# Kernel optimization log

Hardware: AMD Instinct MI355X
Metric: run time of the kernel (lower is better)

Reference implementation:

```python
import jax, jax.numpy as jnp
import numpy as np

N_FP, N_WORD, DIM, LAYERS = 100000, 10000, 32, 3
N_ATOMS, N_WORDS_SEQ = 8192, 4096


def setup_inputs() -> dict:
    key = jax.random.key(0)
    ks = jax.random.split(key, 7)
    return {
        "fingerprints": jax.random.randint(ks[0], (N_ATOMS,), 0, N_FP),
        "adjacency": jax.random.uniform(ks[1], (N_ATOMS, N_ATOMS), dtype=jnp.float32),
        "words": jax.random.randint(ks[2], (N_WORDS_SEQ,), 0, N_WORD),
        "emb_fp": jax.random.normal(ks[3], (N_FP, DIM), dtype=jnp.float32) * 0.02,
        "emb_word": jax.random.normal(ks[4], (N_WORD, DIM), dtype=jnp.float32) * 0.02,
        "Wg": jax.random.normal(ks[5], (LAYERS, DIM, DIM), dtype=jnp.float32) / np.sqrt(DIM),
        "bg": jax.random.normal(ks[6], (LAYERS, DIM), dtype=jnp.float32) * 0.01,
    }


def reference(fingerprints, adjacency, words, emb_fp, emb_word, Wg, bg):
    # Compound vector with GNN: xs <- xs + A @ relu(xs @ W_i + b_i), per layer.
    xs = emb_fp[fingerprints]  # [N, dim]

    def layer(x, wb):
        W, b = wb
        hs = jax.nn.relu(x @ W + b)          # [N, dim]
        return x + adjacency @ hs, None      # dense adjacency matmul + residual

    xs, _ = jax.lax.scan(layer, xs, (Wg, bg))
    compound_vector = xs[None]               # [1, N, dim] (torch.unsqueeze(xs, 0))

    # Protein word embedding lookup (encoder/decoder are external modules).
    word_vectors = emb_word[words]           # [S, dim]
    return compound_vector, word_vectors
```

## Files before the change

kernel.cpp:

```cpp
#include <hip/hip_runtime.h>
#include <hip/hip_bf16.h>
#include <cstdint>
#include <cstddef>

#define NATOMS 8192
#define DIM 32
#define NSEQ 4096
#define KSPLIT 16
#define BM 256
#define BK 32
#define KPB (NATOMS / KSPLIT)
#define NT (KPB / BK)

typedef __attribute__((address_space(1))) const void GV;
typedef __attribute__((address_space(3))) void LV;
using bf16x8 = __attribute__((ext_vector_type(8))) short;
using f32x4  = __attribute__((ext_vector_type(4))) float;

__device__ __forceinline__ void async16(void* lds, const void* g) {
  __builtin_amdgcn_global_load_lds((GV*)g, (LV*)lds, 16, 0, 0);
}
__device__ __forceinline__ void async16nt(void* lds, const void* g) {
  __builtin_amdgcn_global_load_lds((GV*)g, (LV*)lds, 16, 0, 2);
}
__device__ __forceinline__ uint32_t pkbf(float lo, float hi) {
  union { __hip_bfloat16 b[2]; uint32_t u; } v;
  v.b[0] = __float2bfloat16(lo);
  v.b[1] = __float2bfloat16(hi);
  return v.u;
}
__device__ __forceinline__ float ubf(ushort u) {
  union { ushort u; __hip_bfloat16 b; } v;
  v.u = u;
  return __bfloat162float(v.b);
}
union U8 { uint32_t u[4]; bf16x8 v; };

__device__ __forceinline__ int aslot(int r, int g) { return g ^ ((r >> 1) & 3); }
__device__ __forceinline__ int hslot(int n, int g) { return g ^ ((n >> 1) & 3); }

__global__ __launch_bounds__(256, 2)
void cpi_gemm1(const float* __restrict__ A, const ushort* __restrict__ hT,
               float* __restrict__ P, ushort* __restrict__ Abf) {
  __shared__ float  Ab[2][BM * BK];
  __shared__ ushort Hb[2][DIM * BK];

  const int tid  = threadIdx.x;
  const int wave = tid >> 6;
  const int lane = tid & 63;
  const int l15  = lane & 15;
  const int l4   = lane >> 4;
  const int rb   = blockIdx.x & 31;
  const int ks   = blockIdx.x >> 5;
  const int row0 = rb * BM;
  const int k0   = ks * KPB;

  f32x4 acc[4][2];
#pragma unroll
  for (int rt = 0; rt < 4; ++rt)
#pragma unroll
    for (int ct = 0; ct < 2; ++ct) acc[rt][ct] = {0.f, 0.f, 0.f, 0.f};

  auto stage = [&](int buf, int t) {
    const int kb = k0 + t * BK;
#pragma unroll
    for (int i = 0; i < 8; ++i) {
      const int D = (wave * 8 + i) * 64 + lane;
      const int r = D >> 3;
      const int c = D & 7;
      const float* src =
          A + (size_t)(row0 + r) * NATOMS + kb + ((c ^ (r & 7)) << 2);
      async16nt(&Ab[buf][(wave * 8 + i) * 256], src);
    }
    if (wave < 2) {
      const int E = wave * 64 + lane;
      const int n = E >> 2;
      const int s = E & 3;
      const ushort* src = hT + (size_t)n * NATOMS + kb + (hslot(n, s) << 3);
      async16(&Hb[buf][wave * 512], src);
    }
  };

  stage(0, 0);
  asm volatile("s_waitcnt vmcnt(0)" ::: "memory");
  __syncthreads();

  int cur = 0;
#pragma unroll 1
  for (int t = 0; t < NT; ++t) {
    if (t + 1 < NT) stage(cur ^ 1, t + 1);

    const float*  Ac = &Ab[cur][0];
    const ushort* Hc = &Hb[cur][0];

    bf16x8 av[4];
#pragma unroll
    for (int rt = 0; rt < 4; ++rt) {
      const int r = wave * 64 + rt * 16 + l15;
      const float4 f0 =
          *(const float4*)(Ac + r * 32 + (((2 * l4) ^ (r & 7)) << 2));
      const float4 f1 =
          *(const float4*)(Ac + r * 32 + (((2 * l4 + 1) ^ (r & 7)) << 2));
      U8 u;
      u.u[0] = pkbf(f0.x, f0.y);
      u.u[1] = pkbf(f0.z, f0.w);
      u.u[2] = pkbf(f1.x, f1.y);
      u.u[3] = pkbf(f1.z, f1.w);
      av[rt] = u.v;
    }
    bf16x8 bv[2];
#pragma unroll
    for (int ct = 0; ct < 2; ++ct) {
      const int n = ct * 16 + l15;
      bv[ct] = *(const bf16x8*)(Hc + n * 32 + (hslot(n, l4) << 3));
    }

    ushort* Tb = Abf + (((size_t)ks * 32 + rb) * 16 + t) * (BM * BK);
#pragma unroll
    for (int rt = 0; rt < 4; ++rt) {
      const int r = wave * 64 + rt * 16 + l15;
      *(bf16x8*)(Tb + r * 32 + (aslot(r, l4) << 3)) = av[rt];
    }

#pragma unroll
    for (int rt = 0; rt < 4; ++rt)
#pragma unroll
      for (int ct = 0; ct < 2; ++ct)
        acc[rt][ct] = __builtin_amdgcn_mfma_f32_16x16x32_bf16(
            av[rt], bv[ct], acc[rt][ct], 0, 0, 0);

    asm volatile("s_waitcnt vmcnt(4)" ::: "memory");
    __syncthreads();
    cur ^= 1;
  }

  float* Pp = P + ((((size_t)ks * 32 + rb) * 4 + wave) * 8) * 256;
#pragma unroll
  for (int rt = 0; rt < 4; ++rt)
#pragma unroll
    for (int ct = 0; ct < 2; ++ct)
      *(f32x4*)(Pp + (rt * 2 + ct) * 256 + lane * 4) = acc[rt][ct];
}

__global__ __launch_bounds__(256, 2)
void cpi_gemm2(const ushort* __restrict__ Abf, const ushort* __restrict__ hT,
               ushort* __restrict__ Pb, const int ntA) {
  __shared__ ushort Ab[3][BM * BK];
  __shared__ ushort Hb[3][DIM * BK];

  const int tid  = threadIdx.x;
  const int wave = tid >> 6;
  const int lane = tid & 63;
  const int l15  = lane & 15;
  const int l4   = lane >> 4;
  const int rb   = blockIdx.x & 31;
  const int ks   = blockIdx.x >> 5;
  const int k0   = ks * KPB;

  f32x4 acc[4][2];
#pragma unroll
  for (int rt = 0; rt < 4; ++rt)
#pragma unroll
    for (int ct = 0; ct < 2; ++ct) acc[rt][ct] = {0.f, 0.f, 0.f, 0.f};

  auto stage = [&](int buf, int t) {
    const ushort* Tb = Abf + (((size_t)ks * 32 + rb) * 16 + t) * (BM * BK);
#pragma unroll
    for (int i = 0; i < 4; ++i) {
      const ushort* src = Tb + ((wave * 4 + i) * 64 + lane) * 8;
      void* dst = &Ab[buf][(wave * 4 + i) * 512];
      if (ntA)
        async16nt(dst, src);
      else
        async16(dst, src);
    }
    if (wave < 2) {
      const int kb = k0 + t * BK;
      const int E = wave * 64 + lane;
      const int n = E >> 2;
      const int s = E & 3;
      const ushort* src = hT + (size_t)n * NATOMS + kb + (hslot(n, s) << 3);
      async16(&Hb[buf][wave * 512], src);
    }
  };

  stage(0, 0);
  stage(1, 1);

#pragma unroll 1
  for (int t = 0; t < NT; ++t) {
    if (t + 1 < NT) {
      if (wave < 2)
        asm volatile("s_waitcnt vmcnt(5)" ::: "memory");
      else
        asm volatile("s_waitcnt vmcnt(4)" ::: "memory");
    } else {
      asm volatile("s_waitcnt vmcnt(0)" ::: "memory");
    }
    __syncthreads();
    if (t + 2 < NT) stage((t + 2) % 3, t + 2);

    const ushort* Ac = &Ab[t % 3][0];
    const ushort* Hc = &Hb[t % 3][0];

    bf16x8 av[4], bv[2];
#pragma unroll
    for (int rt = 0; rt < 4; ++rt) {
      const int r = wave * 64 + rt * 16 + l15;
      av[rt] = *(const bf16x8*)(Ac + r * 32 + (aslot(r, l4) << 3));
    }
#pragma unroll
    for (int ct = 0; ct < 2; ++ct) {
      const int n = ct * 16 + l15;
      bv[ct] = *(const bf16x8*)(Hc + n * 32 + (hslot(n, l4) << 3));
    }

#pragma unroll
    for (int rt = 0; rt < 4; ++rt)
#pragma unroll
      for (int ct = 0; ct < 2; ++ct)
        acc[rt][ct] = __builtin_amdgcn_mfma_f32_16x16x32_bf16(
            av[rt], bv[ct], acc[rt][ct], 0, 0, 0);
  }

  ushort* Pp = Pb + ((((size_t)ks * 32 + rb) * 4 + wave) * 8) * 256;
#pragma unroll
  for (int rt = 0; rt < 4; ++rt)
#pragma unroll
    for (int ct = 0; ct < 2; ++ct) {
      uint2 u;
      u.x = pkbf(acc[rt][ct].x, acc[rt][ct].y);
      u.y = pkbf(acc[rt][ct].z, acc[rt][ct].w);
      *(uint2*)(Pp + (rt * 2 + ct) * 256 + lane * 4) = u;
    }
}

__global__ __launch_bounds__(256)
void cpi_front(const int* __restrict__ fp, const float* __restrict__ embfp,
               const float* __restrict__ W, const float* __restrict__ b,
               float* __restrict__ xs, ushort* __restrict__ hT,
               const int* __restrict__ words, const float* __restrict__ embw,
               float* __restrict__ wout) {
  if (blockIdx.x >= NATOMS / 8) {
    const int i = (blockIdx.x - NATOMS / 8) * 256 + threadIdx.x;
    wout[i] = embw[(size_t)words[i >> 5] * DIM + (i & 31)];
    return;
  }
  __shared__ float xsl[8][DIM];
  __shared__ float Wl[DIM][DIM];
  const int tid = threadIdx.x;
  const int col = tid & 31;
  const int r8  = tid >> 5;
  const int row = blockIdx.x * 8 + r8;
  const int f   = fp[row];
  const float v = embfp[(size_t)f * DIM + col];
  xs[(size_t)row * DIM + col] = v;
  xsl[r8][col] = v;
#pragma unroll
  for (int i = 0; i < 4; ++i) {
    const int idx = tid + i * 256;
    ((float*)Wl)[idx] = W[idx];
  }
  __syncthreads();
  float a = b[col];
#pragma unroll
  for (int d = 0; d < DIM; ++d) a += xsl[r8][d] * Wl[d][col];
  union { __hip_bfloat16 bb; ushort u; } cv;
  cv.bb = __float2bfloat16(fmaxf(a, 0.f));
  hT[(size_t)col * NATOMS + row] = cv.u;
}

__global__ __launch_bounds__(256)
void cpi_reduce_h(const float* __restrict__ P, const ushort* __restrict__ Pb,
                  const int p_is_bf16, const float* __restrict__ W,
                  const float* __restrict__ b, float* __restrict__ xs,
                  ushort* __restrict__ hT, const int compute_h) {
  __shared__ float xsl[8][DIM];
  __shared__ float Wl[DIM][DIM];
  const int tid = threadIdx.x;
  const int col = tid & 31;
  const int r8  = tid >> 5;
  const int row = blockIdx.x * 8 + r8;
  const size_t off = (size_t)row * DIM + col;
  float s = xs[off];
  {
    const int rbv = row >> 8, rr = row & 255;
    const int w = rr >> 6, rr6 = rr & 63;
    const int rt = rr6 >> 4, q4 = (rr6 >> 2) & 3, i = rr6 & 3;
    const int ct = col >> 4, lane = q4 * 16 + (col & 15);
    const int base = ((rbv * 4 + w) * 8 + rt * 2 + ct) * 256 + lane * 4 + i;
    if (p_is_bf16) {
#pragma unroll
      for (int k = 0; k < KSPLIT; ++k)
        s += ubf(Pb[(size_t)k * (NATOMS * DIM) + base]);
    } else {
#pragma unroll
      for (int k = 0; k < KSPLIT; ++k)
        s += __builtin_nontemporal_load(&P[(size_t)k * (NATOMS * DIM) + base]);
    }
  }
  xs[off] = s;
  if (compute_h) {
    xsl[r8][col] = s;
#pragma unroll
    for (int i = 0; i < 4; ++i) {
      const int idx = tid + i * 256;
      ((float*)Wl)[idx] = W[idx];
    }
    __syncthreads();
    float a = b[col];
#pragma unroll
    for (int d = 0; d < DIM; ++d) a += xsl[r8][d] * Wl[d][col];
    union { __hip_bfloat16 bb; ushort u; } cv;
    cv.bb = __float2bfloat16(fmaxf(a, 0.f));
    hT[(size_t)col * NATOMS + row] = cv.u;
  }
}

extern "C" void kernel_launch(void* const* d_in, const int* in_sizes, int n_in,
                              void* d_out, int out_size, void* d_ws, size_t ws_size,
                              hipStream_t stream) {
  const int*   fp    = (const int*)d_in[0];
  const float* adj   = (const float*)d_in[1];
  const int*   words = (const int*)d_in[2];
  const float* embfp = (const float*)d_in[3];
  const float* embw  = (const float*)d_in[4];
  const float* Wg    = (const float*)d_in[5];
  const float* bg    = (const float*)d_in[6];

  float* out = (float*)d_out;
  float* xs  = out;
  float* wv  = out + NATOMS * DIM;

  float*  P   = (float*)d_ws;
  ushort* Pb  = (ushort*)P;
  ushort* Abf = (ushort*)(P + (size_t)KSPLIT * NATOMS * DIM);
  ushort* hT  = Abf + (size_t)NATOMS * NATOMS;

  cpi_front<<<dim3(NATOMS / 8 + NSEQ * DIM / 256), dim3(256), 0, stream>>>(
      fp, embfp, Wg, bg, xs, hT, words, embw, wv);

  cpi_gemm1<<<dim3(512), dim3(256), 0, stream>>>(adj, hT, P, Abf);
  cpi_reduce_h<<<dim3(NATOMS / 8), dim3(256), 0, stream>>>(
      P, Pb, 0, Wg + DIM * DIM, bg + DIM, xs, hT, 1);

  cpi_gemm2<<<dim3(512), dim3(256), 0, stream>>>(Abf, hT, Pb, 0);
  cpi_reduce_h<<<dim3(NATOMS / 8), dim3(256), 0, stream>>>(
      P, Pb, 1, Wg + 2 * DIM * DIM, bg + 2 * DIM, xs, hT, 1);

  cpi_gemm2<<<dim3(512), dim3(256), 0, stream>>>(Abf, hT, Pb, 1);
  cpi_reduce_h<<<dim3(NATOMS / 8), dim3(256), 0, stream>>>(
      P, Pb, 1, Wg, bg, xs, hT, 0);
}
```

Measured before the change: 141.4 us.

## Fuse split-K reduction and next-layer h compute into GEMM via last-block atomics

Removes the three separate reduce_h launches. Each GEMM block now bumps a per-row-block atomic counter, and the last of the KSPLIT blocks for that row block sums the partials, updates xs, and computes the next layer's relu(xW+b) into a ping-pong hT buffer. This saves launch overhead and the extra pass over the partials, but leaves the reduction tail to only 32 blocks, which serialises that work. Counters are zeroed by an extra block in the front kernel.

```diff
diff --git a/kernel.cpp b/kernel.cpp
--- a/kernel.cpp
+++ b/kernel.cpp
@@ -11,11 +11,13 @@
 #define BK 32
 #define KPB (NATOMS / KSPLIT)
 #define NT (KPB / BK)
+#define FRONT_NB (NATOMS / 8 + NSEQ * DIM / 256)
 
 typedef __attribute__((address_space(1))) const void GV;
 typedef __attribute__((address_space(3))) void LV;
 using bf16x8 = __attribute__((ext_vector_type(8))) short;
 using f32x4  = __attribute__((ext_vector_type(4))) float;
+using u32x2  = __attribute__((ext_vector_type(2))) unsigned int;
 
 __device__ __forceinline__ void async16(void* lds, const void* g) {
   __builtin_amdgcn_global_load_lds((GV*)g, (LV*)lds, 16, 0, 0);
@@ -34,16 +36,48 @@
   v.u = u;
   return __bfloat162float(v.b);
 }
+__device__ __forceinline__ ushort bfr(float a) {
+  union { __hip_bfloat16 b; ushort u; } v;
+  v.b = __float2bfloat16(a);
+  return v.u;
+}
 union U8 { uint32_t u[4]; bf16x8 v; };
 
 __device__ __forceinline__ int aslot(int r, int g) { return g ^ ((r >> 1) & 3); }
 __device__ __forceinline__ int hslot(int n, int g) { return g ^ ((n >> 1) & 3); }
 
+__device__ __forceinline__ void h_tail(const float* xsl, const float* Wl,
+                                       const float* bn, ushort* hTout,
+                                       int row0, int tid) {
+  float wcol[DIM];
+  const int c = tid & 31;
+#pragma unroll
+  for (int d = 0; d < DIM; ++d) wcol[d] = Wl[d * DIM + c];
+  const float bb = bn[c];
+#pragma unroll 1
+  for (int it = 0; it < 32; ++it) {
+    const int r = it * 8 + (tid >> 5);
+    float a = bb;
+    const f32x4* xr = (const f32x4*)(xsl + r * DIM);
+#pragma unroll
+    for (int q = 0; q < 8; ++q) {
+      f32x4 x4 = xr[q];
+      a += x4.x * wcol[q * 4] + x4.y * wcol[q * 4 + 1] +
+           x4.z * wcol[q * 4 + 2] + x4.w * wcol[q * 4 + 3];
+    }
+    hTout[(size_t)c * NATOMS + row0 + r] = bfr(fmaxf(a, 0.f));
+  }
+}
+
 __global__ __launch_bounds__(256, 2)
-void cpi_gemm1(const float* __restrict__ A, const ushort* __restrict__ hT,
-               float* __restrict__ P, ushort* __restrict__ Abf) {
+void cpi_gemm1(const float* __restrict__ A, const ushort* __restrict__ hTin,
+               float* __restrict__ P, ushort* __restrict__ Abf,
+               int* __restrict__ cnt, const float* __restrict__ Wn,
+               const float* __restrict__ bn, float* __restrict__ xs,
+               ushort* __restrict__ hTout) {
   __shared__ float  Ab[2][BM * BK];
   __shared__ ushort Hb[2][DIM * BK];
+  __shared__ int lastFlag;
 
   const int tid  = threadIdx.x;
   const int wave = tid >> 6;
@@ -76,7 +110,7 @@
       const int E = wave * 64 + lane;
       const int n = E >> 2;
       const int s = E & 3;
-      const ushort* src = hT + (size_t)n * NATOMS + kb + (hslot(n, s) << 3);
+      const ushort* src = hTin + (size_t)n * NATOMS + kb + (hslot(n, s) << 3);
       async16(&Hb[buf][wave * 512], src);
     }
   };
@@ -140,13 +174,59 @@
 #pragma unroll
     for (int ct = 0; ct < 2; ++ct)
       *(f32x4*)(Pp + (rt * 2 + ct) * 256 + lane * 4) = acc[rt][ct];
+
+  asm volatile("s_waitcnt vmcnt(0)" ::: "memory");
+  __syncthreads();
+  if (tid == 0) {
+    int c = __hip_atomic_fetch_add(&cnt[rb], 1, __ATOMIC_ACQ_REL,
+                                   __HIP_MEMORY_SCOPE_AGENT);
+    lastFlag = (c == KSPLIT - 1);
+  }
+  __syncthreads();
+  if (!lastFlag) return;
+
+  float* xsl = (float*)&Ab[0][0];
+  float* Wl  = xsl + 256 * DIM;
+  for (int i = tid; i < DIM * DIM; i += 256) Wl[i] = Wn[i];
+
+  const int colq = lane & 15, rq = lane >> 4;
+#pragma unroll
+  for (int f = 0; f < 8; ++f) {
+    const size_t base = ((size_t)(rb * 4 + wave) * 8 + f) * 256 + lane * 4;
+    const int rt = f >> 1, ct = f & 1;
+    f32x4 a4;
+#pragma unroll
+    for (int i = 0; i < 4; ++i) {
+      const int row = wave * 64 + rt * 16 + rq * 4 + i;
+      a4[i] = xs[(size_t)(row0 + row) * DIM + ct * 16 + colq];
+    }
+#pragma unroll
+    for (int k = 0; k < KSPLIT; ++k) {
+      f32x4 v = __builtin_nontemporal_load(
+          (const f32x4*)(P + (size_t)k * (NATOMS * DIM) + base));
+      a4.x += v.x; a4.y += v.y; a4.z += v.z; a4.w += v.w;
+    }
+#pragma unroll
+    for (int i = 0; i < 4; ++i) {
+      const int row = wave * 64 + rt * 16 + rq * 4 + i;
+      const int col = ct * 16 + colq;
+      xs[(size_t)(row0 + row) * DIM + col] = a4[i];
+      xsl[row * DIM + col] = a4[i];
+    }
+  }
+  __syncthreads();
+  h_tail(xsl, Wl, bn, hTout, row0, tid);
 }
 
 __global__ __launch_bounds__(256, 2)
-void cpi_gemm2(const ushort* __restrict__ Abf, const ushort* __restrict__ hT,
-               ushort* __restrict__ Pb, const int ntA) {
+void cpi_gemm2(const ushort* __restrict__ Abf, const ushort* __restrict__ hTin,
+               ushort* __restrict__ Pb, const int ntA, int* __restrict__ cnt,
+               const float* __restrict__ Wn, const float* __restrict__ bn,
+               float* __restrict__ xs, ushort* __restrict__ hTout,
+               const int doH) {
   __shared__ ushort Ab[3][BM * BK];
   __shared__ ushort Hb[3][DIM * BK];
+  __shared__ int lastFlag;
 
   const int tid  = threadIdx.x;
   const int wave = tid >> 6;
@@ -155,6 +235,7 @@
   const int l4   = lane >> 4;
   const int rb   = blockIdx.x & 31;
   const int ks   = blockIdx.x >> 5;
+  const int row0 = rb * BM;
   const int k0   = ks * KPB;
 
   f32x4 acc[4][2];
@@ -179,7 +260,7 @@
       const int E = wave * 64 + lane;
       const int n = E >> 2;
       const int s = E & 3;
-      const ushort* src = hT + (size_t)n * NATOMS + kb + (hslot(n, s) << 3);
+      const ushort* src = hTin + (size_t)n * NATOMS + kb + (hslot(n, s) << 3);
       async16(&Hb[buf][wave * 512], src);
     }
   };
@@ -228,11 +309,59 @@
   for (int rt = 0; rt < 4; ++rt)
 #pragma unroll
     for (int ct = 0; ct < 2; ++ct) {
-      uint2 u;
+      u32x2 u;
       u.x = pkbf(acc[rt][ct].x, acc[rt][ct].y);
       u.y = pkbf(acc[rt][ct].z, acc[rt][ct].w);
-      *(uint2*)(Pp + (rt * 2 + ct) * 256 + lane * 4) = u;
-    }
+      *(u32x2*)(Pp + (rt * 2 + ct) * 256 + lane * 4) = u;
+    }
+
+  asm volatile("s_waitcnt vmcnt(0)" ::: "memory");
+  __syncthreads();
+  if (tid == 0) {
+    int c = __hip_atomic_fetch_add(&cnt[rb], 1, __ATOMIC_ACQ_REL,
+                                   __HIP_MEMORY_SCOPE_AGENT);
+    lastFlag = (c == KSPLIT - 1);
+  }
+  __syncthreads();
+  if (!lastFlag) return;
+
+  float* xsl = (float*)&Ab[0][0];
+  float* Wl  = xsl + 256 * DIM;
+  if (doH)
+    for (int i = tid; i < DIM * DIM; i += 256) Wl[i] = Wn[i];
+
+  const int colq = lane & 15, rq = lane >> 4;
+#pragma unroll
+  for (int f = 0; f < 8; ++f) {
+    const size_t base = ((size_t)(rb * 4 + wave) * 8 + f) * 256 + lane * 4;
+    const int rt = f >> 1, ct = f & 1;
+    f32x4 a4;
+#pragma unroll
+    for (int i = 0; i < 4; ++i) {
+      const int row = wave * 64 + rt * 16 + rq * 4 + i;
+      a4[i] = xs[(size_t)(row0 + row) * DIM + ct * 16 + colq];
+    }
+#pragma unroll
+    for (int k = 0; k < KSPLIT; ++k) {
+      u32x2 v = __builtin_nontemporal_load(
+          (const u32x2*)(Pb + (size_t)k * (NATOMS * DIM) + base));
+      a4.x += ubf((ushort)(v.x & 0xffff));
+      a4.y += ubf((ushort)(v.x >> 16));
+      a4.z += ubf((ushort)(v.y & 0xffff));
+      a4.w += ubf((ushort)(v.y >> 16));
+    }
+#pragma unroll
+    for (int i = 0; i < 4; ++i) {
+      const int row = wave * 64 + rt * 16 + rq * 4 + i;
+      const int col = ct * 16 + colq;
+      xs[(size_t)(row0 + row) * DIM + col] = a4[i];
+      if (doH) xsl[row * DIM + col] = a4[i];
+    }
+  }
+  if (doH) {
+    __syncthreads();
+    h_tail(xsl, Wl, bn, hTout, row0, tid);
+  }
 }
 
 __global__ __launch_bounds__(256)
@@ -240,7 +369,11 @@
                const float* __restrict__ W, const float* __restrict__ b,
                float* __restrict__ xs, ushort* __restrict__ hT,
                const int* __restrict__ words, const float* __restrict__ embw,
-               float* __restrict__ wout) {
+               float* __restrict__ wout, int* __restrict__ cnt) {
+  if (blockIdx.x == FRONT_NB) {
+    if (threadIdx.x < 96) cnt[threadIdx.x] = 0;
+    return;
+  }
   if (blockIdx.x >= NATOMS / 8) {
     const int i = (blockIdx.x - NATOMS / 8) * 256 + threadIdx.x;
     wout[i] = embw[(size_t)words[i >> 5] * DIM + (i & 31)];
@@ -265,56 +398,7 @@
   float a = b[col];
 #pragma unroll
   for (int d = 0; d < DIM; ++d) a += xsl[r8][d] * Wl[d][col];
-  union { __hip_bfloat16 bb; ushort u; } cv;
-  cv.bb = __float2bfloat16(fmaxf(a, 0.f));
-  hT[(size_t)col * NATOMS + row] = cv.u;
-}
-
-__global__ __launch_bounds__(256)
-void cpi_reduce_h(const float* __restrict__ P, const ushort* __restrict__ Pb,
-                  const int p_is_bf16, const float* __restrict__ W,
-                  const float* __restrict__ b, float* __restrict__ xs,
-                  ushort* __restrict__ hT, const int compute_h) {
-  __shared__ float xsl[8][DIM];
-  __shared__ float Wl[DIM][DIM];
-  const int tid = threadIdx.x;
-  const int col = tid & 31;
-  const int r8  = tid >> 5;
-  const int row = blockIdx.x * 8 + r8;
-  const size_t off = (size_t)row * DIM + col;
-  float s = xs[off];
-  {
-    const int rbv = row >> 8, rr = row & 255;
-    const int w = rr >> 6, rr6 = rr & 63;
-    const int rt = rr6 >> 4, q4 = (rr6 >> 2) & 3, i = rr6 & 3;
-    const int ct = col >> 4, lane = q4 * 16 + (col & 15);
-    const int base = ((rbv * 4 + w) * 8 + rt * 2 + ct) * 256 + lane * 4 + i;
-    if (p_is_bf16) {
-#pragma unroll
-      for (int k = 0; k < KSPLIT; ++k)
-        s += ubf(Pb[(size_t)k * (NATOMS * DIM) + base]);
-    } else {
-#pragma unroll
-      for (int k = 0; k < KSPLIT; ++k)
-        s += __builtin_nontemporal_load(&P[(size_t)k * (NATOMS * DIM) + base]);
-    }
-  }
-  xs[off] = s;
-  if (compute_h) {
-    xsl[r8][col] = s;
-#pragma unroll
-    for (int i = 0; i < 4; ++i) {
-      const int idx = tid + i * 256;
-      ((float*)Wl)[idx] = W[idx];
-    }
-    __syncthreads();
-    float a = b[col];
-#pragma unroll
-    for (int d = 0; d < DIM; ++d) a += xsl[r8][d] * Wl[d][col];
-    union { __hip_bfloat16 bb; ushort u; } cv;
-    cv.bb = __float2bfloat16(fmaxf(a, 0.f));
-    hT[(size_t)col * NATOMS + row] = cv.u;
-  }
+  hT[(size_t)col * NATOMS + row] = bfr(fmaxf(a, 0.f));
 }
 
 extern "C" void kernel_launch(void* const* d_in, const int* in_sizes, int n_in,
@@ -335,20 +419,19 @@
   float*  P   = (float*)d_ws;
   ushort* Pb  = (ushort*)P;
   ushort* Abf = (ushort*)(P + (size_t)KSPLIT * NATOMS * DIM);
-  ushort* hT  = Abf + (size_t)NATOMS * NATOMS;
-
-  cpi_front<<<dim3(NATOMS / 8 + NSEQ * DIM / 256), dim3(256), 0, stream>>>(
-      fp, embfp, Wg, bg, xs, hT, words, embw, wv);
-
-  cpi_gemm1<<<dim3(512), dim3(256), 0, stream>>>(adj, hT, P, Abf);
-  cpi_reduce_h<<<dim3(NATOMS / 8), dim3(256), 0, stream>>>(
-      P, Pb, 0, Wg + DIM * DIM, bg + DIM, xs, hT, 1);
-
-  cpi_gemm2<<<dim3(512), dim3(256), 0, stream>>>(Abf, hT, Pb, 0);
-  cpi_reduce_h<<<dim3(NATOMS / 8), dim3(256), 0, stream>>>(
-      P, Pb, 1, Wg + 2 * DIM * DIM, bg + 2 * DIM, xs, hT, 1);
-
-  cpi_gemm2<<<dim3(512), dim3(256), 0, stream>>>(Abf, hT, Pb, 1);
-  cpi_reduce_h<<<dim3(NATOMS / 8), dim3(256), 0, stream>>>(
-      P, Pb, 1, Wg, bg, xs, hT, 0);
-}
+  ushort* hTa = Abf + (size_t)NATOMS * NATOMS;
+  ushort* hTb = hTa + (size_t)DIM * NATOMS;
+  int*    cnt = (int*)(hTb + (size_t)DIM * NATOMS);
+
+  cpi_front<<<dim3(FRONT_NB + 1), dim3(256), 0, stream>>>(
+      fp, embfp, Wg, bg, xs, hTa, words, embw, wv, cnt);
+
+  cpi_gemm1<<<dim3(512), dim3(256), 0, stream>>>(
+      adj, hTa, P, Abf, cnt, Wg + DIM * DIM, bg + DIM, xs, hTb);
+
+  cpi_gemm2<<<dim3(512), dim3(256), 0, stream>>>(
+      Abf, hTb, Pb, 0, cnt + 32, Wg + 2 * DIM * DIM, bg + 2 * DIM, xs, hTa, 1);
+
+  cpi_gemm2<<<dim3(512), dim3(256), 0, stream>>>(
+      Abf, hTa, Pb, 1, cnt + 64, Wg, bg, xs, hTb, 0);
+}
```

New measurement: 201.1 us. 1.42x slower.

## Fuse all GNN layers into one persistent kernel with grid barriers

Applied to the files above, without the earlier changes.

Replaces the seven kernel launches (front, gemm1, gemm2 and the reduce kernels) with one persistent 512-block kernel. Software grid barriers built on atomics separate the phases. Each block keeps its own xs rows in registers across the reduce phases, and hT is double-buffered so a phase never overwrites the hT it is reading. This is meant to remove launch gaps and the xs round trips through global memory. The risks are that all 512 blocks must be co-resident (two per CU) or the barrier deadlocks, each barrier adds spin and atomic cost, and the large shared buffer may limit occupancy.

```diff
diff --git a/kernel.cpp b/kernel.cpp
--- a/kernel.cpp
+++ b/kernel.cpp
@@ -11,11 +11,13 @@
 #define BK 32
 #define KPB (NATOMS / KSPLIT)
 #define NT (KPB / BK)
+#define NBLK 512
 
 typedef __attribute__((address_space(1))) const void GV;
 typedef __attribute__((address_space(3))) void LV;
 using bf16x8 = __attribute__((ext_vector_type(8))) short;
 using f32x4  = __attribute__((ext_vector_type(4))) float;
+using u32x2  = __attribute__((ext_vector_type(2))) unsigned int;
 
 __device__ __forceinline__ void async16(void* lds, const void* g) {
   __builtin_amdgcn_global_load_lds((GV*)g, (LV*)lds, 16, 0, 0);
@@ -34,129 +36,38 @@
   v.u = u;
   return __bfloat162float(v.b);
 }
+__device__ __forceinline__ ushort bfr(float a) {
+  union { __hip_bfloat16 b; ushort u; } v;
+  v.b = __float2bfloat16(a);
+  return v.u;
+}
 union U8 { uint32_t u[4]; bf16x8 v; };
 
 __device__ __forceinline__ int aslot(int r, int g) { return g ^ ((r >> 1) & 3); }
 __device__ __forceinline__ int hslot(int n, int g) { return g ^ ((n >> 1) & 3); }
 
-__global__ __launch_bounds__(256, 2)
-void cpi_gemm1(const float* __restrict__ A, const ushort* __restrict__ hT,
-               float* __restrict__ P, ushort* __restrict__ Abf) {
-  __shared__ float  Ab[2][BM * BK];
-  __shared__ ushort Hb[2][DIM * BK];
-
-  const int tid  = threadIdx.x;
-  const int wave = tid >> 6;
-  const int lane = tid & 63;
-  const int l15  = lane & 15;
-  const int l4   = lane >> 4;
-  const int rb   = blockIdx.x & 31;
-  const int ks   = blockIdx.x >> 5;
-  const int row0 = rb * BM;
-  const int k0   = ks * KPB;
-
-  f32x4 acc[4][2];
-#pragma unroll
-  for (int rt = 0; rt < 4; ++rt)
-#pragma unroll
-    for (int ct = 0; ct < 2; ++ct) acc[rt][ct] = {0.f, 0.f, 0.f, 0.f};
-
-  auto stage = [&](int buf, int t) {
-    const int kb = k0 + t * BK;
-#pragma unroll
-    for (int i = 0; i < 8; ++i) {
-      const int D = (wave * 8 + i) * 64 + lane;
-      const int r = D >> 3;
-      const int c = D & 7;
-      const float* src =
-          A + (size_t)(row0 + r) * NATOMS + kb + ((c ^ (r & 7)) << 2);
-      async16nt(&Ab[buf][(wave * 8 + i) * 256], src);
-    }
-    if (wave < 2) {
-      const int E = wave * 64 + lane;
-      const int n = E >> 2;
-      const int s = E & 3;
-      const ushort* src = hT + (size_t)n * NATOMS + kb + (hslot(n, s) << 3);
-      async16(&Hb[buf][wave * 512], src);
-    }
-  };
-
-  stage(0, 0);
-  asm volatile("s_waitcnt vmcnt(0)" ::: "memory");
+__device__ __forceinline__ void gridbar(int* cnt, int* gen, int tid) {
   __syncthreads();
-
-  int cur = 0;
-#pragma unroll 1
-  for (int t = 0; t < NT; ++t) {
-    if (t + 1 < NT) stage(cur ^ 1, t + 1);
-
-    const float*  Ac = &Ab[cur][0];
-    const ushort* Hc = &Hb[cur][0];
-
-    bf16x8 av[4];
-#pragma unroll
-    for (int rt = 0; rt < 4; ++rt) {
-      const int r = wave * 64 + rt * 16 + l15;
-      const float4 f0 =
-          *(const float4*)(Ac + r * 32 + (((2 * l4) ^ (r & 7)) << 2));
-      const float4 f1 =
-          *(const float4*)(Ac + r * 32 + (((2 * l4 + 1) ^ (r & 7)) << 2));
-      U8 u;
-      u.u[0] = pkbf(f0.x, f0.y);
-      u.u[1] = pkbf(f0.z, f0.w);
-      u.u[2] = pkbf(f1.x, f1.y);
-      u.u[3] = pkbf(f1.z, f1.w);
-      av[rt] = u.v;
-    }
-    bf16x8 bv[2];
-#pragma unroll
-    for (int ct = 0; ct < 2; ++ct) {
-      const int n = ct * 16 + l15;
-      bv[ct] = *(const bf16x8*)(Hc + n * 32 + (hslot(n, l4) << 3));
-    }
-
-    ushort* Tb = Abf + (((size_t)ks * 32 + rb) * 16 + t) * (BM * BK);
-#pragma unroll
-    for (int rt = 0; rt < 4; ++rt) {
-      const int r = wave * 64 + rt * 16 + l15;
-      *(bf16x8*)(Tb + r * 32 + (aslot(r, l4) << 3)) = av[rt];
-    }
-
-#pragma unroll
-    for (int rt = 0; rt < 4; ++rt)
-#pragma unroll
-      for (int ct = 0; ct < 2; ++ct)
-        acc[rt][ct] = __builtin_amdgcn_mfma_f32_16x16x32_bf16(
-            av[rt], bv[ct], acc[rt][ct], 0, 0, 0);
-
-    asm volatile("s_waitcnt vmcnt(4)" ::: "memory");
-    __syncthreads();
-    cur ^= 1;
-  }
-
-  float* Pp = P + ((((size_t)ks * 32 + rb) * 4 + wave) * 8) * 256;
-#pragma unroll
-  for (int rt = 0; rt < 4; ++rt)
-#pragma unroll
-    for (int ct = 0; ct < 2; ++ct)
-      *(f32x4*)(Pp + (rt * 2 + ct) * 256 + lane * 4) = acc[rt][ct];
-}
-
-__global__ __launch_bounds__(256, 2)
-void cpi_gemm2(const ushort* __restrict__ Abf, const ushort* __restrict__ hT,
-               ushort* __restrict__ Pb, const int ntA) {
-  __shared__ ushort Ab[3][BM * BK];
-  __shared__ ushort Hb[3][DIM * BK];
-
-  const int tid  = threadIdx.x;
-  const int wave = tid >> 6;
-  const int lane = tid & 63;
-  const int l15  = lane & 15;
-  const int l4   = lane >> 4;
-  const int rb   = blockIdx.x & 31;
-  const int ks   = blockIdx.x >> 5;
-  const int k0   = ks * KPB;
-
+  if (tid == 0) {
+    int g = __hip_atomic_load(gen, __ATOMIC_RELAXED, __HIP_MEMORY_SCOPE_AGENT);
+    if (__hip_atomic_fetch_add(cnt, 1, __ATOMIC_ACQ_REL,
+                               __HIP_MEMORY_SCOPE_AGENT) == NBLK - 1) {
+      __hip_atomic_store(cnt, 0, __ATOMIC_RELAXED, __HIP_MEMORY_SCOPE_AGENT);
+      __hip_atomic_store(gen, g ^ 1, __ATOMIC_RELEASE,
+                         __HIP_MEMORY_SCOPE_AGENT);
+    } else {
+      while (__hip_atomic_load(gen, __ATOMIC_ACQUIRE,
+                               __HIP_MEMORY_SCOPE_AGENT) == g)
+        __builtin_amdgcn_s_sleep(8);
+    }
+  }
+  __syncthreads();
+}
+
+__device__ __forceinline__ void gemm2_body(
+    const ushort* __restrict__ Abf, const ushort* __restrict__ hTin,
+    ushort* __restrict__ Pb, int ntA, ushort* AbB, ushort* HbU, int tid,
+    int wave, int lane, int l15, int l4, int rb, int ks, int k0) {
   f32x4 acc[4][2];
 #pragma unroll
   for (int rt = 0; rt < 4; ++rt)
@@ -168,7 +79,7 @@
 #pragma unroll
     for (int i = 0; i < 4; ++i) {
       const ushort* src = Tb + ((wave * 4 + i) * 64 + lane) * 8;
-      void* dst = &Ab[buf][(wave * 4 + i) * 512];
+      void* dst = AbB + buf * 8192 + (wave * 4 + i) * 512;
       if (ntA)
         async16nt(dst, src);
       else
@@ -179,8 +90,8 @@
       const int E = wave * 64 + lane;
       const int n = E >> 2;
       const int s = E & 3;
-      const ushort* src = hT + (size_t)n * NATOMS + kb + (hslot(n, s) << 3);
-      async16(&Hb[buf][wave * 512], src);
+      const ushort* src = hTin + (size_t)n * NATOMS + kb + (hslot(n, s) << 3);
+      async16(HbU + buf * 1024 + wave * 512, src);
     }
   };
 
@@ -200,8 +111,8 @@
     __syncthreads();
     if (t + 2 < NT) stage((t + 2) % 3, t + 2);
 
-    const ushort* Ac = &Ab[t % 3][0];
-    const ushort* Hc = &Hb[t % 3][0];
+    const ushort* Ac = AbB + (t % 3) * 8192;
+    const ushort* Hc = HbU + (t % 3) * 1024;
 
     bf16x8 av[4], bv[2];
 #pragma unroll
@@ -228,68 +139,32 @@
   for (int rt = 0; rt < 4; ++rt)
 #pragma unroll
     for (int ct = 0; ct < 2; ++ct) {
-      uint2 u;
+      u32x2 u;
       u.x = pkbf(acc[rt][ct].x, acc[rt][ct].y);
       u.y = pkbf(acc[rt][ct].z, acc[rt][ct].w);
-      *(uint2*)(Pp + (rt * 2 + ct) * 256 + lane * 4) = u;
-    }
-}
-
-__global__ __launch_bounds__(256)
-void cpi_front(const int* __restrict__ fp, const float* __restrict__ embfp,
-               const float* __restrict__ W, const float* __restrict__ b,
-               float* __restrict__ xs, ushort* __restrict__ hT,
-               const int* __restrict__ words, const float* __restrict__ embw,
-               float* __restrict__ wout) {
-  if (blockIdx.x >= NATOMS / 8) {
-    const int i = (blockIdx.x - NATOMS / 8) * 256 + threadIdx.x;
-    wout[i] = embw[(size_t)words[i >> 5] * DIM + (i & 31)];
-    return;
-  }
-  __shared__ float xsl[8][DIM];
-  __shared__ float Wl[DIM][DIM];
-  const int tid = threadIdx.x;
+      *(u32x2*)(Pp + (rt * 2 + ct) * 256 + lane * 4) = u;
+    }
+}
+
+__device__ __forceinline__ void reduce_body(
+    const float* __restrict__ P, const ushort* __restrict__ Pb, int isbf,
+    const float* __restrict__ Wn, const float* __restrict__ bn,
+    ushort* __restrict__ hTout, int doH, float* xsr, float* xsl, float* Wl,
+    int row0r, int tid) {
   const int col = tid & 31;
-  const int r8  = tid >> 5;
-  const int row = blockIdx.x * 8 + r8;
-  const int f   = fp[row];
-  const float v = embfp[(size_t)f * DIM + col];
-  xs[(size_t)row * DIM + col] = v;
-  xsl[r8][col] = v;
-#pragma unroll
-  for (int i = 0; i < 4; ++i) {
-    const int idx = tid + i * 256;
-    ((float*)Wl)[idx] = W[idx];
-  }
-  __syncthreads();
-  float a = b[col];
-#pragma unroll
-  for (int d = 0; d < DIM; ++d) a += xsl[r8][d] * Wl[d][col];
-  union { __hip_bfloat16 bb; ushort u; } cv;
-  cv.bb = __float2bfloat16(fmaxf(a, 0.f));
-  hT[(size_t)col * NATOMS + row] = cv.u;
-}
-
-__global__ __launch_bounds__(256)
-void cpi_reduce_h(const float* __restrict__ P, const ushort* __restrict__ Pb,
-                  const int p_is_bf16, const float* __restrict__ W,
-                  const float* __restrict__ b, float* __restrict__ xs,
-                  ushort* __restrict__ hT, const int compute_h) {
-  __shared__ float xsl[8][DIM];
-  __shared__ float Wl[DIM][DIM];
-  const int tid = threadIdx.x;
-  const int col = tid & 31;
-  const int r8  = tid >> 5;
-  const int row = blockIdx.x * 8 + r8;
-  const size_t off = (size_t)row * DIM + col;
-  float s = xs[off];
-  {
-    const int rbv = row >> 8, rr = row & 255;
-    const int w = rr >> 6, rr6 = rr & 63;
+  if (doH)
+    for (int i = tid; i < DIM * DIM; i += 256) Wl[i] = Wn[i];
+#pragma unroll
+  for (int rr = 0; rr < 2; ++rr) {
+    const int lr = (tid >> 5) + rr * 8;
+    const int row = row0r + lr;
+    const int rbv = row >> 8, r255 = row & 255;
+    const int w = r255 >> 6, rr6 = r255 & 63;
     const int rt = rr6 >> 4, q4 = (rr6 >> 2) & 3, i = rr6 & 3;
     const int ct = col >> 4, lane = q4 * 16 + (col & 15);
     const int base = ((rbv * 4 + w) * 8 + rt * 2 + ct) * 256 + lane * 4 + i;
-    if (p_is_bf16) {
+    float s = xsr[rr];
+    if (isbf) {
 #pragma unroll
       for (int k = 0; k < KSPLIT; ++k)
         s += ubf(Pb[(size_t)k * (NATOMS * DIM) + base]);
@@ -298,22 +173,192 @@
       for (int k = 0; k < KSPLIT; ++k)
         s += __builtin_nontemporal_load(&P[(size_t)k * (NATOMS * DIM) + base]);
     }
-  }
-  xs[off] = s;
-  if (compute_h) {
-    xsl[r8][col] = s;
-#pragma unroll
-    for (int i = 0; i < 4; ++i) {
-      const int idx = tid + i * 256;
-      ((float*)Wl)[idx] = W[idx];
-    }
+    xsr[rr] = s;
+    if (doH) xsl[lr * DIM + col] = s;
+  }
+  if (doH) {
     __syncthreads();
-    float a = b[col];
-#pragma unroll
-    for (int d = 0; d < DIM; ++d) a += xsl[r8][d] * Wl[d][col];
-    union { __hip_bfloat16 bb; ushort u; } cv;
-    cv.bb = __float2bfloat16(fmaxf(a, 0.f));
-    hT[(size_t)col * NATOMS + row] = cv.u;
+    float wc[DIM];
+#pragma unroll
+    for (int d = 0; d < DIM; ++d) wc[d] = Wl[d * DIM + col];
+    const float bb = bn[col];
+#pragma unroll
+    for (int rr = 0; rr < 2; ++rr) {
+      const int lr = (tid >> 5) + rr * 8;
+      float a = bb;
+#pragma unroll
+      for (int d = 0; d < DIM; ++d) a += xsl[lr * DIM + d] * wc[d];
+      hTout[(size_t)col * NATOMS + row0r + lr] = bfr(fmaxf(a, 0.f));
+    }
+  }
+}
+
+__global__ __launch_bounds__(256, 2)
+void cpi_mega(const int* __restrict__ fp, const float* __restrict__ adj,
+              const int* __restrict__ words, const float* __restrict__ embfp,
+              const float* __restrict__ embw, const float* __restrict__ Wg,
+              const float* __restrict__ bg, float* __restrict__ out,
+              float* __restrict__ P, ushort* __restrict__ Pb,
+              ushort* __restrict__ Abf, ushort* __restrict__ hTa,
+              ushort* __restrict__ hTb, int* __restrict__ bar) {
+  __shared__ __align__(16) char smem[71680];
+  float*  AbF = (float*)smem;
+  ushort* AbB = (ushort*)smem;
+  ushort* HbU = (ushort*)(smem + 65536);
+  float*  xsl = (float*)smem;
+  float*  Wl  = (float*)(smem + 4096);
+
+  const int tid   = threadIdx.x;
+  const int bid   = blockIdx.x;
+  const int wave  = tid >> 6;
+  const int lane  = tid & 63;
+  const int l15   = lane & 15;
+  const int l4    = lane >> 4;
+  const int rb    = bid & 31;
+  const int ks    = bid >> 5;
+  const int row0g = rb * BM;
+  const int k0    = ks * KPB;
+  const int row0r = bid * 16;
+  const int col   = tid & 31;
+
+  float xsr[2];
+
+  {
+    const int wi = bid * 256 + tid;
+    out[NATOMS * DIM + wi] = embw[(size_t)words[wi >> 5] * DIM + (wi & 31)];
+    for (int i = tid; i < DIM * DIM; i += 256) Wl[i] = Wg[i];
+#pragma unroll
+    for (int rr = 0; rr < 2; ++rr) {
+      const int lr = (tid >> 5) + rr * 8;
+      const float v = embfp[(size_t)fp[row0r + lr] * DIM + col];
+      xsr[rr] = v;
+      xsl[lr * DIM + col] = v;
+    }
+    __syncthreads();
+    float wc[DIM];
+#pragma unroll
+    for (int d = 0; d < DIM; ++d) wc[d] = Wl[d * DIM + col];
+    const float bb = bg[col];
+#pragma unroll
+    for (int rr = 0; rr < 2; ++rr) {
+      const int lr = (tid >> 5) + rr * 8;
+      float a = bb;
+#pragma unroll
+      for (int d = 0; d < DIM; ++d) a += xsl[lr * DIM + d] * wc[d];
+      hTa[(size_t)col * NATOMS + row0r + lr] = bfr(fmaxf(a, 0.f));
+    }
+  }
+  gridbar(bar, bar + 1, tid);
+
+  {
+    f32x4 acc[4][2];
+#pragma unroll
+    for (int rt = 0; rt < 4; ++rt)
+#pragma unroll
+      for (int ct = 0; ct < 2; ++ct) acc[rt][ct] = {0.f, 0.f, 0.f, 0.f};
+
+    auto stage = [&](int buf, int t) {
+      const int kb = k0 + t * BK;
+#pragma unroll
+      for (int i = 0; i < 8; ++i) {
+        const int D = (wave * 8 + i) * 64 + lane;
+        const int r = D >> 3;
+        const int c = D & 7;
+        const float* src =
+            adj + (size_t)(row0g + r) * NATOMS + kb + ((c ^ (r & 7)) << 2);
+        async16nt(AbF + buf * 8192 + (wave * 8 + i) * 256, src);
+      }
+      if (wave < 2) {
+        const int E = wave * 64 + lane;
+        const int n = E >> 2;
+        const int s = E & 3;
+        const ushort* src =
+            hTa + (size_t)n * NATOMS + kb + (hslot(n, s) << 3);
+        async16(HbU + buf * 1024 + wave * 512, src);
+      }
+    };
+
+    stage(0, 0);
+    asm volatile("s_waitcnt vmcnt(0)" ::: "memory");
+    __syncthreads();
+
+    int cur = 0;
+#pragma unroll 1
+    for (int t = 0; t < NT; ++t) {
+      if (t + 1 < NT) stage(cur ^ 1, t + 1);
+
+      const float*  Ac = AbF + cur * 8192;
+      const ushort* Hc = HbU + cur * 1024;
+
+      bf16x8 av[4];
+#pragma unroll
+      for (int rt = 0; rt < 4; ++rt) {
+        const int r = wave * 64 + rt * 16 + l15;
+        const float4 f0 =
+            *(const float4*)(Ac + r * 32 + (((2 * l4) ^ (r & 7)) << 2));
+        const float4 f1 =
+            *(const float4*)(Ac + r * 32 + (((2 * l4 + 1) ^ (r & 7)) << 2));
+        U8 u;
+        u.u[0] = pkbf(f0.x, f0.y);
+        u.u[1] = pkbf(f0.z, f0.w);
+        u.u[2] = pkbf(f1.x, f1.y);
+        u.u[3] = pkbf(f1.z, f1.w);
+        av[rt] = u.v;
+      }
+      bf16x8 bv[2];
+#pragma unroll
+      for (int ct = 0; ct < 2; ++ct) {
+        const int n = ct * 16 + l15;
+        bv[ct] = *(const bf16x8*)(Hc + n * 32 + (hslot(n, l4) << 3));
+      }
+
+      ushort* Tb = Abf + (((size_t)ks * 32 + rb) * 16 + t) * (BM * BK);
+#pragma unroll
+      for (int rt = 0; rt < 4; ++rt) {
+        const int r = wave * 64 + rt * 16 + l15;
+        *(bf16x8*)(Tb + r * 32 + (aslot(r, l4) << 3)) = av[rt];
+      }
+
+#pragma unroll
+      for (int rt = 0; rt < 4; ++rt)
+#pragma unroll
+        for (int ct = 0; ct < 2; ++ct)
+          acc[rt][ct] = __builtin_amdgcn_mfma_f32_16x16x32_bf16(
+              av[rt], bv[ct], acc[rt][ct], 0, 0, 0);
+
+      asm volatile("s_waitcnt vmcnt(4)" ::: "memory");
+      __syncthreads();
+      cur ^= 1;
+    }
+
+    float* Pp = P + ((((size_t)ks * 32 + rb) * 4 + wave) * 8) * 256;
+#pragma unroll
+    for (int rt = 0; rt < 4; ++rt)
+#pragma unroll
+      for (int ct = 0; ct < 2; ++ct)
+        *(f32x4*)(Pp + (rt * 2 + ct) * 256 + lane * 4) = acc[rt][ct];
+  }
+  gridbar(bar, bar + 1, tid);
+
+  reduce_body(P, Pb, 0, Wg + DIM * DIM, bg + DIM, hTb, 1, xsr, xsl, Wl,
+              row0r, tid);
+  gridbar(bar, bar + 1, tid);
+
+  gemm2_body(Abf, hTb, Pb, 0, AbB, HbU, tid, wave, lane, l15, l4, rb, ks, k0);
+  gridbar(bar, bar + 1, tid);
+
+  reduce_body(P, Pb, 1, Wg + 2 * DIM * DIM, bg + 2 * DIM, hTa, 1, xsr, xsl,
+              Wl, row0r, tid);
+  gridbar(bar, bar + 1, tid);
+
+  gemm2_body(Abf, hTa, Pb, 1, AbB, HbU, tid, wave, lane, l15, l4, rb, ks, k0);
+  gridbar(bar, bar + 1, tid);
+
+  reduce_body(P, Pb, 1, Wg, bg, hTb, 0, xsr, xsl, Wl, row0r, tid);
+#pragma unroll
+  for (int rr = 0; rr < 2; ++rr) {
+    const int lr = (tid >> 5) + rr * 8;
+    out[(size_t)(row0r + lr) * DIM + col] = xsr[rr];
   }
 }
 
@@ -329,26 +374,15 @@
   const float* bg    = (const float*)d_in[6];
 
   float* out = (float*)d_out;
-  float* xs  = out;
-  float* wv  = out + NATOMS * DIM;
 
   float*  P   = (float*)d_ws;
   ushort* Pb  = (ushort*)P;
   ushort* Abf = (ushort*)(P + (size_t)KSPLIT * NATOMS * DIM);
-  ushort* hT  = Abf + (size_t)NATOMS * NATOMS;
-
-  cpi_front<<<dim3(NATOMS / 8 + NSEQ * DIM / 256), dim3(256), 0, stream>>>(
-      fp, embfp, Wg, bg, xs, hT, words, embw, wv);
-
-  cpi_gemm1<<<dim3(512), dim3(256), 0, stream>>>(adj, hT, P, Abf);
-  cpi_reduce_h<<<dim3(NATOMS / 8), dim3(256), 0, stream>>>(
-      P, Pb, 0, Wg + DIM * DIM, bg + DIM, xs, hT, 1);
-
-  cpi_gemm2<<<dim3(512), dim3(256), 0, stream>>>(Abf, hT, Pb, 0);
-  cpi_reduce_h<<<dim3(NATOMS / 8), dim3(256), 0, stream>>>(
-      P, Pb, 1, Wg + 2 * DIM * DIM, bg + 2 * DIM, xs, hT, 1);
-
-  cpi_gemm2<<<dim3(512), dim3(256), 0, stream>>>(Abf, hT, Pb, 1);
-  cpi_reduce_h<<<dim3(NATOMS / 8), dim3(256), 0, stream>>>(
-      P, Pb, 1, Wg, bg, xs, hT, 0);
-}
+  ushort* hTa = Abf + (size_t)NATOMS * NATOMS;
+  ushort* hTb = hTa + (size_t)DIM * NATOMS;
+  int*    bar = (int*)(hTb + (size_t)DIM * NATOMS);
+
+  hipMemsetAsync(bar, 0, 8, stream);
+  cpi_mega<<<dim3(NBLK), dim3(256), 0, stream>>>(
+      fp, adj, words, embfp, embw, Wg, bg, out, P, Pb, Abf, hTa, hTb, bar);
+}
```

Measured after the change: 550.0 us. +288.8%, slower.
